# Performance work log

Hardware: AMD Instinct MI355X
Metric: run time of the kernel (lower is better)

## Reference

```python
import jax, jax.numpy as jnp
import numpy as np

QUANTSCALE = 0.25
EPS = 1e-5

def act_quant(x):
    # 8-bit symmetric activation quantization, scale per last dim (as in BitNetMCU)
    scale = 127.0 / jnp.maximum(jnp.max(jnp.abs(x), axis=-1, keepdims=True), EPS)
    return jnp.clip(jnp.round(x * scale), -128.0, 127.0) / scale

def wq_binary(w):
    # Binary weights: sign(w - mean) scaled by mean(|w|) (per-tensor)
    scale = jnp.mean(jnp.abs(w))
    return jnp.sign(w - jnp.mean(w)) * scale

def wq_4bitsym(w):
    # 4-bit symmetric levels {+-0.5,...,+-7.5}/scale, per-tensor scale from mean(|w|)
    mag = jnp.maximum(jnp.mean(jnp.abs(w)), EPS)
    scale = QUANTSCALE * 8.0 / mag
    return (jnp.clip(jnp.round(w * scale - 0.5), -8.0, 7.0) + 0.5) / scale

def ste(x, q):
    # straight-through estimator: forward = q, backward = identity
    return x + jax.lax.stop_gradient(q - x)

def rmsnorm(x):
    return x * jax.lax.rsqrt(jnp.mean(x * x, axis=-1, keepdims=True) + EPS)

def bitlinear(x, w):
    xn = rmsnorm(x)                    # NormType='RMS'
    xq = ste(xn, act_quant(xn))
    wq = ste(w, wq_binary(w))          # QuantType='Binary'
    return xq @ wq.T

def bitconv(x, w, groups):
    # NormType='None', QuantType='4bitsym'
    xq = ste(x, act_quant(x))
    wq = ste(w, wq_4bitsym(w))
    return jax.lax.conv_general_dilated(
        xq, wq, window_strides=(1, 1), padding='VALID',
        dimension_numbers=('NCHW', 'OIHW', 'NCHW'),
        feature_group_count=groups)

def setup_inputs() -> dict:
    key = jax.random.key(0)
    ks = jax.random.split(key, 8)
    B, W1, W2, W3 = 16384, 512, 512, 512
    return {
        'x':        jax.random.normal(ks[0], (B, 1, 16, 16), jnp.float32),
        'conv1_w':  jax.random.normal(ks[1], (16, 1, 3, 3), jnp.float32) * 0.1,
        'conv1b_w': jax.random.normal(ks[2], (16, 1, 3, 3), jnp.float32) * 0.1,
        'conv2_w':  jax.random.normal(ks[3], (96, 1, 12, 12), jnp.float32) * 0.1,
        'fc1_w':    jax.random.normal(ks[4], (W1, 96), jnp.float32) * 0.1,
        'fc2_w':    jax.random.normal(ks[5], (W2, W1), jnp.float32) * 0.1,
        'fc3_w':    jax.random.normal(ks[6], (W3, W2), jnp.float32) * 0.1,
        'fcl_w':    jax.random.normal(ks[7], (10, W3), jnp.float32) * 0.1,
    }

def reference(x, conv1_w, conv1b_w, conv2_w, fc1_w, fc2_w, fc3_w, fcl_w):
    h = jax.nn.relu(bitconv(x, conv1_w, 1))    # [B,16,14,14]
    h = jax.nn.relu(bitconv(h, conv1b_w, 16))  # depthwise -> [B,16,12,12]
    h = jax.nn.relu(bitconv(h, conv2_w, 16))   # grouped k12 -> [B,96,1,1]
    h = h.reshape(h.shape[0], -1)              # [B,96]
    h = jax.nn.relu(bitlinear(h, fc1_w))
    h = jax.nn.relu(bitlinear(h, fc2_w))
    h = jax.nn.relu(bitlinear(h, fc3_w))
    return bitlinear(h, fcl_w)                 # [B,10] logits (dropout is eval no-op)
```

## Files before the change

kernel.cpp:

```cpp
#include <hip/hip_runtime.h>
#include <math.h>

#define EPSQ 1e-5

typedef int v4i  __attribute__((ext_vector_type(4)));
typedef int v16i __attribute__((ext_vector_type(16)));

__device__ void bstat(const float* __restrict__ w, int cnt, double2* dst, int divn) {
    __shared__ double ls[4], la[4];
    int t = threadIdx.x;
    double s = 0.0, a = 0.0;
    const float4* w4 = (const float4*)w;
    int nv = cnt >> 2;
    for (int i = t; i < nv; i += 256) {
        float4 v = w4[i];
        s += (double)v.x + (double)v.y + (double)v.z + (double)v.w;
        a += fabs((double)v.x) + fabs((double)v.y) + fabs((double)v.z) + fabs((double)v.w);
    }
    for (int o = 32; o; o >>= 1) { s += __shfl_down(s, o); a += __shfl_down(a, o); }
    if ((t & 63) == 0) { ls[t >> 6] = s; la[t >> 6] = a; }
    __syncthreads();
    if (t == 0) {
        for (int i = 1; i < 4; i++) { s += ls[i]; a += la[i]; }
        if (divn > 0) { dst->x = s / divn; dst->y = a / divn; }
        else          { dst->x = s;        dst->y = a; }
    }
}

__global__ __launch_bounds__(256) void wstats_part(
    const float* __restrict__ a0, const float* __restrict__ a1,
    const float* __restrict__ a2, const float* __restrict__ a3,
    const float* __restrict__ a4, const float* __restrict__ a5,
    const float* __restrict__ a6, double2* __restrict__ part,
    double2* __restrict__ stats) {
    int b = blockIdx.x;
    if      (b == 0) bstat(a0, 144,   stats + 0, 144);
    else if (b == 1) bstat(a1, 144,   stats + 1, 144);
    else if (b == 2) bstat(a2, 13824, stats + 2, 13824);
    else if (b == 3) bstat(a6, 5120,  stats + 6, 5120);
    else if (b < 8)  bstat(a3 + (b - 4)  * 12288, 12288, part + (b - 4), 0);
    else if (b < 24) bstat(a4 + (b - 8)  * 16384, 16384, part + 4 + (b - 8), 0);
    else             bstat(a5 + (b - 24) * 16384, 16384, part + 20 + (b - 24), 0);
}

__global__ __launch_bounds__(64) void wstats_comb(const double2* __restrict__ part,
                                                  double2* __restrict__ stats) {
    int t = threadIdx.x;
    if (t == 0) {
        double s = 0, a = 0;
        for (int i = 0; i < 4; i++) { s += part[i].x; a += part[i].y; }
        stats[3].x = s / 49152.0; stats[3].y = a / 49152.0;
    } else if (t == 1) {
        double s = 0, a = 0;
        for (int i = 4; i < 20; i++) { s += part[i].x; a += part[i].y; }
        stats[4].x = s / 262144.0; stats[4].y = a / 262144.0;
    } else if (t == 2) {
        double s = 0, a = 0;
        for (int i = 20; i < 36; i++) { s += part[i].x; a += part[i].y; }
        stats[5].x = s / 262144.0; stats[5].y = a / 262144.0;
    }
}

__device__ inline float q4odd(float w, double mag) {
    double sc = 2.0 / fmax(mag, EPSQ);
    double q = fmin(fmax(rint((double)w * sc - 0.5), -8.0), 7.0);
    return (float)(2.0 * q + 1.0);
}

__global__ __launch_bounds__(256) void wq_conv(
    const float* __restrict__ wc1, const float* __restrict__ wc1b,
    const float* __restrict__ wc2, const double2* __restrict__ stats,
    float* __restrict__ c1o, float* __restrict__ c1bo, float* __restrict__ c2o) {
    int i = blockIdx.x * 256 + threadIdx.x;
    if (i < 144) c1o[i] = q4odd(wc1[i], stats[0].y);
    else if (i < 288) c1bo[i - 144] = q4odd(wc1b[i - 144], stats[1].y);
    else if (i < 288 + 13824) { int j = i - 288; c2o[j] = q4odd(wc2[j], stats[2].y); }
}

__device__ inline char bsign(float w, double mean) {
    double d = (double)w - mean;
    return d > 0.0 ? (char)1 : (d < 0.0 ? (char)-1 : (char)0);
}

__global__ __launch_bounds__(256) void wq_fc(
    const float* __restrict__ wfc1, const float* __restrict__ wfc2,
    const float* __restrict__ wfc3, const float* __restrict__ wfcl,
    const double2* __restrict__ stats,
    char* __restrict__ f1, char* __restrict__ f2,
    char* __restrict__ f3, char* __restrict__ fl) {
    int i = blockIdx.x * 256 + threadIdx.x;
    if (i < 65536) {
        int row = i >> 7, k = i & 127;
        f1[i] = (k < 96) ? bsign(wfc1[row * 96 + k], stats[3].x) : (char)0;
        return;
    }
    i -= 65536;
    if (i < 262144) { f2[i] = bsign(wfc2[i], stats[4].x); return; }
    i -= 262144;
    if (i < 262144) { f3[i] = bsign(wfc3[i], stats[5].x); return; }
    i -= 262144;
    if (i < 5120)   { fl[i] = bsign(wfcl[i], stats[6].x); }
}

template <int Wd>
__device__ inline double cpix(const float (&rq)[3][Wd], const float* wv,
                              const double* inv, int qx) {
    float d0 = rq[0][qx] * wv[0] + rq[0][qx + 1] * wv[1] + rq[0][qx + 2] * wv[2];
    float d1 = rq[1][qx] * wv[3] + rq[1][qx + 1] * wv[4] + rq[1][qx + 2] * wv[5];
    float d2 = rq[2][qx] * wv[6] + rq[2][qx + 1] * wv[7] + rq[2][qx + 2] * wv[8];
    return (double)d0 * inv[0] + (double)d1 * inv[1] + (double)d2 * inv[2];
}

__global__ __launch_bounds__(256) void conv_fused(
    const float* __restrict__ x, const float* __restrict__ w1o,
    const float* __restrict__ w1bo, const float* __restrict__ w2o,
    const double2* __restrict__ stats,
    char* __restrict__ xq96, double* __restrict__ arow) {
    __shared__ float sxp[16][17];
    __shared__ double sinv0[16];
    __shared__ float sh1[16][14][15];
    __shared__ double sinv1[16][14];
    __shared__ float sh2[16][12][13];
    __shared__ double sinv2[16][12];
    __shared__ float sw1[144], sw1b[144];
    __shared__ double sh3p[2][96];
    __shared__ double sh3[96];
    __shared__ double srs[2];
    int b = blockIdx.x, t = threadIdx.x;
    double cw1  = fmax(stats[0].y, EPSQ) * 0.25;
    double cw1b = fmax(stats[1].y, EPSQ) * 0.25;
    double cw2  = fmax(stats[2].y, EPSQ) * 0.25;

    float v = x[(size_t)b * 256 + t];
    if (t < 144) { sw1[t] = w1o[t]; sw1b[t] = w1bo[t]; }
    float m = fabsf(v);
    for (int o = 8; o; o >>= 1) m = fmaxf(m, __shfl_xor(m, o));
    double s0 = 127.0 / fmax((double)m, EPSQ);
    sxp[t >> 4][t & 15] = (float)fmin(fmax(rint((double)v * s0), -128.0), 127.0);
    if ((t & 15) == 0) sinv0[t >> 4] = 1.0 / s0;
    __syncthreads();

    if (t < 224) {
        int c = t / 14, r = t % 14;
        float rq[3][16]; double inv[3];
        #pragma unroll
        for (int i = 0; i < 3; i++) {
            inv[i] = sinv0[r + i];
            #pragma unroll
            for (int j = 0; j < 16; j++) rq[i][j] = sxp[r + i][j];
        }
        float wv[9];
        #pragma unroll
        for (int k = 0; k < 9; k++) wv[k] = sw1[c * 9 + k];
        double vals[14]; double mx = 0.0;
        #pragma unroll
        for (int qx = 0; qx < 14; qx++) {
            vals[qx] = fmax(cpix(rq, wv, inv, qx) * cw1, 0.0);
            mx = fmax(mx, vals[qx]);
        }
        double s2 = 127.0 / fmax(mx, EPSQ);
        sinv1[c][r] = 1.0 / s2;
        #pragma unroll
        for (int qx = 0; qx < 14; qx++)
            sh1[c][r][qx] = (float)fmin(fmax(rint(vals[qx] * s2), -128.0), 127.0);
    }
    __syncthreads();

    if (t < 192) {
        int c = t / 12, r = t % 12;
        float rq[3][14]; double inv[3];
        #pragma unroll
        for (int i = 0; i < 3; i++) {
            inv[i] = sinv1[c][r + i];
            #pragma unroll
            for (int j = 0; j < 14; j++) rq[i][j] = sh1[c][r + i][j];
        }
        float wv[9];
        #pragma unroll
        for (int k = 0; k < 9; k++) wv[k] = sw1b[c * 9 + k];
        double vals[12]; double mx = 0.0;
        #pragma unroll
        for (int qx = 0; qx < 12; qx++) {
            vals[qx] = fmax(cpix(rq, wv, inv, qx) * cw1b, 0.0);
            mx = fmax(mx, vals[qx]);
        }
        double s3 = 127.0 / fmax(mx, EPSQ);
        sinv2[c][r] = 1.0 / s3;
        #pragma unroll
        for (int qx = 0; qx < 12; qx++)
            sh2[c][r][qx] = (float)fmin(fmax(rint(vals[qx] * s3), -128.0), 127.0);
    }
    __syncthreads();

    if (t < 192) {
        int o = t % 96, half = t / 96;
        int g = o / 6;
        const float* wk = w2o + o * 144 + half * 72;
        double acc = 0.0;
        #pragma unroll
        for (int hh = 0; hh < 6; hh++) {
            int row = half * 6 + hh;
            float4 w0 = *(const float4*)(wk + hh * 12);
            float4 w1 = *(const float4*)(wk + hh * 12 + 4);
            float4 w2v = *(const float4*)(wk + hh * 12 + 8);
            const float* sr = &sh2[g][row][0];
            float d = 0.f;
            d += sr[0] * w0.x; d += sr[1] * w0.y; d += sr[2] * w0.z; d += sr[3] * w0.w;
            d += sr[4] * w1.x; d += sr[5] * w1.y; d += sr[6] * w1.z; d += sr[7] * w1.w;
            d += sr[8] * w2v.x; d += sr[9] * w2v.y; d += sr[10] * w2v.z; d += sr[11] * w2v.w;
            acc += (double)d * sinv2[g][row];
        }
        sh3p[half][o] = acc;
    }
    __syncthreads();
    if (t < 96) sh3[t] = fmax((sh3p[0][t] + sh3p[1][t]) * cw2, 0.0);
    __syncthreads();

    if (t < 64) {
        double a = sh3[t];
        double bb = (t < 32) ? sh3[64 + t] : 0.0;
        double ss = a * a + bb * bb;
        double mxx = fmax(fabs(a), fabs(bb));
        for (int o = 32; o; o >>= 1) {
            ss += __shfl_down(ss, o);
            mxx = fmax(mxx, __shfl_down(mxx, o));
        }
        if (t == 0) {
            double r = 1.0 / sqrt(ss / 96.0 + 1e-5);
            double s4 = 127.0 / fmax(mxx * r, EPSQ);
            srs[0] = r; srs[1] = s4;
        }
    }
    __syncthreads();
    if (t < 128) {
        char q = 0;
        if (t < 96) {
            double xn = sh3[t] * srs[0];
            q = (char)(int)fmin(fmax(rint(xn * srs[1]), -128.0), 127.0);
        }
        xq96[(size_t)b * 128 + t] = q;
        if (t == 0) arow[b] = 1.0 / srs[1];
    }
}

__global__ __launch_bounds__(256) void gemm_i8(
    const char* __restrict__ Xq, const char* __restrict__ Wq,
    int* __restrict__ h, int N, int K, int dorelu) {
    __shared__ char As[16384];
    __shared__ char Bs[16384];
    int t = threadIdx.x;
    int lane = t & 63;
    int w = t >> 6, wr = w >> 1, wc = w & 1;
    int m0 = blockIdx.y * 128, n0 = blockIdx.x * 128;

    v16i acc[2][2] = {};

    for (int k0 = 0; k0 < K; k0 += 128) {
        #pragma unroll
        for (int p = 0; p < 4; p++) {
            int slot = p * 256 + t;
            int row = slot >> 3;
            int cb = (slot & 7) * 16;
            int4 va = *(const int4*)(Xq + (size_t)(m0 + row) * K + k0 + cb);
            int4 vb = *(const int4*)(Wq + (size_t)(n0 + row) * K + k0 + cb);
            int dst = row * 128 + (cb ^ ((row & 7) << 4));
            *(int4*)(As + dst) = va;
            *(int4*)(Bs + dst) = vb;
        }
        __syncthreads();
        int ra0 = wr * 64 + (lane & 31);
        int rb0 = wc * 64 + (lane & 31);
        int ksel = (lane >> 5) * 16;
        #pragma unroll
        for (int kk = 0; kk < 4; kk++) {
            int kb = kk * 32 + ksel;
            v4i a0 = *(v4i*)(As + ra0 * 128        + (kb ^ ((ra0 & 7) << 4)));
            v4i a1 = *(v4i*)(As + (ra0 + 32) * 128 + (kb ^ ((ra0 & 7) << 4)));
            v4i b0 = *(v4i*)(Bs + rb0 * 128        + (kb ^ ((rb0 & 7) << 4)));
            v4i b1 = *(v4i*)(Bs + (rb0 + 32) * 128 + (kb ^ ((rb0 & 7) << 4)));
            acc[0][0] = __builtin_amdgcn_mfma_i32_32x32x32_i8(a0, b0, acc[0][0], 0, 0, 0);
            acc[0][1] = __builtin_amdgcn_mfma_i32_32x32x32_i8(a0, b1, acc[0][1], 0, 0, 0);
            acc[1][0] = __builtin_amdgcn_mfma_i32_32x32x32_i8(a1, b0, acc[1][0], 0, 0, 0);
            acc[1][1] = __builtin_amdgcn_mfma_i32_32x32x32_i8(a1, b1, acc[1][1], 0, 0, 0);
        }
        __syncthreads();
    }

    #pragma unroll
    for (int mt = 0; mt < 2; mt++) {
        int rbase = m0 + wr * 64 + mt * 32 + 4 * (lane >> 5);
        #pragma unroll
        for (int nt = 0; nt < 2; nt++) {
            int cbase = n0 + wc * 64 + nt * 32 + (lane & 31);
            #pragma unroll
            for (int g = 0; g < 4; g++)
                #pragma unroll
                for (int q = 0; q < 4; q++) {
                    int vv = acc[mt][nt][g * 4 + q];
                    if (dorelu) vv = max(vv, 0);
                    h[(size_t)(rbase + g * 8 + q) * N + cbase] = vv;
                }
        }
    }
}

__global__ __launch_bounds__(256) void rmsq_i8(const int* __restrict__ h,
                                               const double2* __restrict__ stats,
                                               int sidx,
                                               double* __restrict__ arow,
                                               char* __restrict__ xq) {
    __shared__ double wsumd[4];
    __shared__ int wmaxi[4];
    __shared__ double fr[2];
    int b = blockIdx.x, t = threadIdx.x;
    const int* xr = h + (size_t)b * 512;
    int v0 = xr[t], v1 = xr[t + 256];
    double ss = (double)v0 * (double)v0 + (double)v1 * (double)v1;
    int mi = max(abs(v0), abs(v1));
    for (int o = 32; o; o >>= 1) {
        ss += __shfl_down(ss, o);
        mi = max(mi, __shfl_down(mi, o));
    }
    if ((t & 63) == 0) { wsumd[t >> 6] = ss; wmaxi[t >> 6] = mi; }
    __syncthreads();
    if (t == 0) {
        double S = wsumd[0] + wsumd[1] + wsumd[2] + wsumd[3];
        int M = max(max(wmaxi[0], wmaxi[1]), max(wmaxi[2], wmaxi[3]));
        double c = stats[sidx].y * arow[b];
        double mean = S * c * c / 512.0;
        double r = 1.0 / sqrt(mean + 1e-5);
        double s = 127.0 / fmax((double)M * c * r, EPSQ);
        fr[0] = c * r * s;
        fr[1] = s;
    }
    __syncthreads();
    double cs = fr[0];
    char q0 = (char)(int)fmin(fmax(rint((double)v0 * cs), -128.0), 127.0);
    char q1 = (char)(int)fmin(fmax(rint((double)v1 * cs), -128.0), 127.0);
    xq[(size_t)b * 512 + t] = q0;
    xq[(size_t)b * 512 + t + 256] = q1;
    if (t == 0) arow[b] = 1.0 / fr[1];
}

__device__ inline int bdot(int a, int b) {
    int r = ((a << 24) >> 24) * ((b << 24) >> 24);
    r += ((a << 16) >> 24) * ((b << 16) >> 24);
    r += ((a << 8) >> 24) * ((b << 8) >> 24);
    r += (a >> 24) * (b >> 24);
    return r;
}

__global__ __launch_bounds__(256) void fcl_k(const char* __restrict__ Xq,
                                             const char* __restrict__ Wq,
                                             const double* __restrict__ arow,
                                             const double2* __restrict__ stats,
                                             float* __restrict__ out) {
    int gi = blockIdx.x * 256 + threadIdx.x;
    int mrow = gi / 10, n = gi - mrow * 10;
    const int4* xp = (const int4*)(Xq + (size_t)mrow * 512);
    const int4* wp = (const int4*)(Wq + n * 512);
    int acc = 0;
    #pragma unroll 8
    for (int i = 0; i < 32; i++) {
        int4 a = xp[i], b = wp[i];
        acc += bdot(a.x, b.x) + bdot(a.y, b.y) + bdot(a.z, b.z) + bdot(a.w, b.w);
    }
    out[gi] = (float)((double)acc * stats[6].y * arow[mrow]);
}

extern "C" void kernel_launch(void* const* d_in, const int* in_sizes, int n_in,
                              void* d_out, int out_size, void* d_ws, size_t ws_size,
                              hipStream_t stream) {
    const float* x     = (const float*)d_in[0];
    const float* w_c1  = (const float*)d_in[1];
    const float* w_c1b = (const float*)d_in[2];
    const float* w_c2  = (const float*)d_in[3];
    const float* w_fc1 = (const float*)d_in[4];
    const float* w_fc2 = (const float*)d_in[5];
    const float* w_fc3 = (const float*)d_in[6];
    const float* w_fcl = (const float*)d_in[7];
    float* out = (float*)d_out;
    char* wsb = (char*)d_ws;
    const int B = 16384;

    float*   c1o   = (float*)(wsb + 0);
    float*   c1bo  = (float*)(wsb + 1024);
    float*   c2o   = (float*)(wsb + 2048);
    double2* stats = (double2*)(wsb + 57344);
    double2* part  = (double2*)(wsb + 57856);
    char*    f1q   = wsb + 65536;
    char*    f2q   = wsb + 131072;
    char*    f3q   = wsb + 393216;
    char*    flq   = wsb + 655360;
    double*  arow  = (double*)(wsb + 663552);
    char*    xq96  = wsb + 1048576;
    char*    xq512 = wsb + 3145728;
    int*     h     = (int*)(wsb + 11534336);

    wstats_part<<<40, 256, 0, stream>>>(w_c1, w_c1b, w_c2, w_fc1, w_fc2, w_fc3,
                                        w_fcl, part, stats);
    wstats_comb<<<1, 64, 0, stream>>>(part, stats);
    wq_conv<<<56, 256, 0, stream>>>(w_c1, w_c1b, w_c2, stats, c1o, c1bo, c2o);
    wq_fc<<<2324, 256, 0, stream>>>(w_fc1, w_fc2, w_fc3, w_fcl, stats, f1q, f2q, f3q, flq);

    conv_fused<<<B, 256, 0, stream>>>(x, c1o, c1bo, c2o, stats, xq96, arow);

    gemm_i8<<<dim3(4, B / 128), 256, 0, stream>>>(xq96, f1q, h, 512, 128, 1);
    rmsq_i8<<<B, 256, 0, stream>>>(h, stats, 3, arow, xq512);
    gemm_i8<<<dim3(4, B / 128), 256, 0, stream>>>(xq512, f2q, h, 512, 512, 1);
    rmsq_i8<<<B, 256, 0, stream>>>(h, stats, 4, arow, xq512);
    gemm_i8<<<dim3(4, B / 128), 256, 0, stream>>>(xq512, f3q, h, 512, 512, 1);
    rmsq_i8<<<B, 256, 0, stream>>>(h, stats, 5, arow, xq512);
    fcl_k<<<640, 256, 0, stream>>>(xq512, flq, arow, stats, out);
}
```

Before: 292.2 us.

## Fuse int8 FC GEMM with RMSNorm and requantization epilogue per row block

Replaces the separate int8 GEMM plus per-row RMS/quantize kernels with one kernel per layer. Each block computes a full 32x512 output row tile, reduces sum-of-squares and max inside the block, and writes int8 activations directly. This removes the int32 intermediate round trip through global memory and three launches. In exchange every block reloads the whole 512-wide weight tile, occupancy is tied to a 64KB shared buffer, and the layer writes xq512 in place while it is also the input. The change also drops clamps the conv path never needs and folds the conv weight scale into the row inverse scales.

```diff
diff --git a/kernel.cpp b/kernel.cpp
--- a/kernel.cpp
+++ b/kernel.cpp
@@ -136,7 +136,7 @@
     float m = fabsf(v);
     for (int o = 8; o; o >>= 1) m = fmaxf(m, __shfl_xor(m, o));
     double s0 = 127.0 / fmax((double)m, EPSQ);
-    sxp[t >> 4][t & 15] = (float)fmin(fmax(rint((double)v * s0), -128.0), 127.0);
+    sxp[t >> 4][t & 15] = (float)rint((double)v * s0);
     if ((t & 15) == 0) sinv0[t >> 4] = 1.0 / s0;
     __syncthreads();
 
@@ -145,7 +145,7 @@
         float rq[3][16]; double inv[3];
         #pragma unroll
         for (int i = 0; i < 3; i++) {
-            inv[i] = sinv0[r + i];
+            inv[i] = sinv0[r + i] * cw1;
             #pragma unroll
             for (int j = 0; j < 16; j++) rq[i][j] = sxp[r + i][j];
         }
@@ -155,14 +155,14 @@
         double vals[14]; double mx = 0.0;
         #pragma unroll
         for (int qx = 0; qx < 14; qx++) {
-            vals[qx] = fmax(cpix(rq, wv, inv, qx) * cw1, 0.0);
+            vals[qx] = fmax(cpix(rq, wv, inv, qx), 0.0);
             mx = fmax(mx, vals[qx]);
         }
         double s2 = 127.0 / fmax(mx, EPSQ);
         sinv1[c][r] = 1.0 / s2;
         #pragma unroll
         for (int qx = 0; qx < 14; qx++)
-            sh1[c][r][qx] = (float)fmin(fmax(rint(vals[qx] * s2), -128.0), 127.0);
+            sh1[c][r][qx] = (float)rint(vals[qx] * s2);
     }
     __syncthreads();
 
@@ -171,7 +171,7 @@
         float rq[3][14]; double inv[3];
         #pragma unroll
         for (int i = 0; i < 3; i++) {
-            inv[i] = sinv1[c][r + i];
+            inv[i] = sinv1[c][r + i] * cw1b;
             #pragma unroll
             for (int j = 0; j < 14; j++) rq[i][j] = sh1[c][r + i][j];
         }
@@ -181,14 +181,14 @@
         double vals[12]; double mx = 0.0;
         #pragma unroll
         for (int qx = 0; qx < 12; qx++) {
-            vals[qx] = fmax(cpix(rq, wv, inv, qx) * cw1b, 0.0);
+            vals[qx] = fmax(cpix(rq, wv, inv, qx), 0.0);
             mx = fmax(mx, vals[qx]);
         }
         double s3 = 127.0 / fmax(mx, EPSQ);
         sinv2[c][r] = 1.0 / s3;
         #pragma unroll
         for (int qx = 0; qx < 12; qx++)
-            sh2[c][r][qx] = (float)fmin(fmax(rint(vals[qx] * s3), -128.0), 127.0);
+            sh2[c][r][qx] = (float)rint(vals[qx] * s3);
     }
     __syncthreads();
 
@@ -236,110 +236,113 @@
         char q = 0;
         if (t < 96) {
             double xn = sh3[t] * srs[0];
-            q = (char)(int)fmin(fmax(rint(xn * srs[1]), -128.0), 127.0);
+            q = (char)(int)rint(xn * srs[1]);
         }
         xq96[(size_t)b * 128 + t] = q;
         if (t == 0) arow[b] = 1.0 / srs[1];
     }
 }
 
-__global__ __launch_bounds__(256) void gemm_i8(
-    const char* __restrict__ Xq, const char* __restrict__ Wq,
-    int* __restrict__ h, int N, int K, int dorelu) {
-    __shared__ char As[16384];
-    __shared__ char Bs[16384];
+__global__ __launch_bounds__(256, 2) void fc_fused(
+    const char* __restrict__ Xq, const char* __restrict__ Wq, int K,
+    const double2* __restrict__ stats, int sidx,
+    double* __restrict__ arow, char* __restrict__ xq) {
+    __shared__ char As[32 * 128];
+    __shared__ char Bs[512 * 128];
+    __shared__ double redS[4][32];
+    __shared__ int    redM[4][32];
+    __shared__ double csrow[32];
     int t = threadIdx.x;
     int lane = t & 63;
-    int w = t >> 6, wr = w >> 1, wc = w & 1;
-    int m0 = blockIdx.y * 128, n0 = blockIdx.x * 128;
-
-    v16i acc[2][2] = {};
+    int w = t >> 6;
+    int m0 = blockIdx.x * 32;
+
+    v16i acc[4] = {};
 
     for (int k0 = 0; k0 < K; k0 += 128) {
-        #pragma unroll
-        for (int p = 0; p < 4; p++) {
+        {
+            int row = t >> 3, cb = (t & 7) * 16;
+            *(int4*)(As + row * 128 + (cb ^ ((row & 7) << 4))) =
+                *(const int4*)(Xq + (size_t)(m0 + row) * K + k0 + cb);
+        }
+        #pragma unroll
+        for (int p = 0; p < 16; p++) {
             int slot = p * 256 + t;
-            int row = slot >> 3;
-            int cb = (slot & 7) * 16;
-            int4 va = *(const int4*)(Xq + (size_t)(m0 + row) * K + k0 + cb);
-            int4 vb = *(const int4*)(Wq + (size_t)(n0 + row) * K + k0 + cb);
-            int dst = row * 128 + (cb ^ ((row & 7) << 4));
-            *(int4*)(As + dst) = va;
-            *(int4*)(Bs + dst) = vb;
+            int row = slot >> 3, cb = (slot & 7) * 16;
+            *(int4*)(Bs + row * 128 + (cb ^ ((row & 7) << 4))) =
+                *(const int4*)(Wq + (size_t)row * K + k0 + cb);
         }
         __syncthreads();
-        int ra0 = wr * 64 + (lane & 31);
-        int rb0 = wc * 64 + (lane & 31);
+        int ra = lane & 31;
         int ksel = (lane >> 5) * 16;
         #pragma unroll
         for (int kk = 0; kk < 4; kk++) {
             int kb = kk * 32 + ksel;
-            v4i a0 = *(v4i*)(As + ra0 * 128        + (kb ^ ((ra0 & 7) << 4)));
-            v4i a1 = *(v4i*)(As + (ra0 + 32) * 128 + (kb ^ ((ra0 & 7) << 4)));
-            v4i b0 = *(v4i*)(Bs + rb0 * 128        + (kb ^ ((rb0 & 7) << 4)));
-            v4i b1 = *(v4i*)(Bs + (rb0 + 32) * 128 + (kb ^ ((rb0 & 7) << 4)));
-            acc[0][0] = __builtin_amdgcn_mfma_i32_32x32x32_i8(a0, b0, acc[0][0], 0, 0, 0);
-            acc[0][1] = __builtin_amdgcn_mfma_i32_32x32x32_i8(a0, b1, acc[0][1], 0, 0, 0);
-            acc[1][0] = __builtin_amdgcn_mfma_i32_32x32x32_i8(a1, b0, acc[1][0], 0, 0, 0);
-            acc[1][1] = __builtin_amdgcn_mfma_i32_32x32x32_i8(a1, b1, acc[1][1], 0, 0, 0);
+            v4i a = *(v4i*)(As + ra * 128 + (kb ^ ((ra & 7) << 4)));
+            #pragma unroll
+            for (int nt = 0; nt < 4; nt++) {
+                int rb = w * 128 + nt * 32 + (lane & 31);
+                v4i bb = *(v4i*)(Bs + rb * 128 + (kb ^ ((rb & 7) << 4)));
+                acc[nt] = __builtin_amdgcn_mfma_i32_32x32x32_i8(a, bb, acc[nt], 0, 0, 0);
+            }
         }
         __syncthreads();
     }
 
+    double ps[16]; int pm[16];
     #pragma unroll
-    for (int mt = 0; mt < 2; mt++) {
-        int rbase = m0 + wr * 64 + mt * 32 + 4 * (lane >> 5);
-        #pragma unroll
-        for (int nt = 0; nt < 2; nt++) {
-            int cbase = n0 + wc * 64 + nt * 32 + (lane & 31);
-            #pragma unroll
-            for (int g = 0; g < 4; g++)
-                #pragma unroll
-                for (int q = 0; q < 4; q++) {
-                    int vv = acc[mt][nt][g * 4 + q];
-                    if (dorelu) vv = max(vv, 0);
-                    h[(size_t)(rbase + g * 8 + q) * N + cbase] = vv;
-                }
-        }
-    }
-}
-
-__global__ __launch_bounds__(256) void rmsq_i8(const int* __restrict__ h,
-                                               const double2* __restrict__ stats,
-                                               int sidx,
-                                               double* __restrict__ arow,
-                                               char* __restrict__ xq) {
-    __shared__ double wsumd[4];
-    __shared__ int wmaxi[4];
-    __shared__ double fr[2];
-    int b = blockIdx.x, t = threadIdx.x;
-    const int* xr = h + (size_t)b * 512;
-    int v0 = xr[t], v1 = xr[t + 256];
-    double ss = (double)v0 * (double)v0 + (double)v1 * (double)v1;
-    int mi = max(abs(v0), abs(v1));
-    for (int o = 32; o; o >>= 1) {
-        ss += __shfl_down(ss, o);
-        mi = max(mi, __shfl_down(mi, o));
-    }
-    if ((t & 63) == 0) { wsumd[t >> 6] = ss; wmaxi[t >> 6] = mi; }
-    __syncthreads();
-    if (t == 0) {
-        double S = wsumd[0] + wsumd[1] + wsumd[2] + wsumd[3];
-        int M = max(max(wmaxi[0], wmaxi[1]), max(wmaxi[2], wmaxi[3]));
-        double c = stats[sidx].y * arow[b];
+    for (int reg = 0; reg < 16; reg++) {
+        int v0 = max(acc[0][reg], 0), v1 = max(acc[1][reg], 0);
+        int v2 = max(acc[2][reg], 0), v3 = max(acc[3][reg], 0);
+        acc[0][reg] = v0; acc[1][reg] = v1; acc[2][reg] = v2; acc[3][reg] = v3;
+        ps[reg] = (double)v0 * v0 + (double)v1 * v1 + (double)v2 * v2 + (double)v3 * v3;
+        pm[reg] = max(max(v0, v1), max(v2, v3));
+    }
+    #pragma unroll
+    for (int o = 1; o < 32; o <<= 1) {
+        #pragma unroll
+        for (int reg = 0; reg < 16; reg++) {
+            ps[reg] += __shfl_xor(ps[reg], o);
+            pm[reg] = max(pm[reg], __shfl_xor(pm[reg], o));
+        }
+    }
+    if ((lane & 31) == 0) {
+        int h = lane >> 5;
+        #pragma unroll
+        for (int reg = 0; reg < 16; reg++) {
+            int row = (reg & 3) + 8 * (reg >> 2) + 4 * h;
+            redS[w][row] = ps[reg];
+            redM[w][row] = pm[reg];
+        }
+    }
+    __syncthreads();
+    if (t < 32) {
+        double S = redS[0][t] + redS[1][t] + redS[2][t] + redS[3][t];
+        int M = max(max(redM[0][t], redM[1][t]), max(redM[2][t], redM[3][t]));
+        double c = stats[sidx].y * arow[m0 + t];
         double mean = S * c * c / 512.0;
         double r = 1.0 / sqrt(mean + 1e-5);
         double s = 127.0 / fmax((double)M * c * r, EPSQ);
-        fr[0] = c * r * s;
-        fr[1] = s;
-    }
-    __syncthreads();
-    double cs = fr[0];
-    char q0 = (char)(int)fmin(fmax(rint((double)v0 * cs), -128.0), 127.0);
-    char q1 = (char)(int)fmin(fmax(rint((double)v1 * cs), -128.0), 127.0);
-    xq[(size_t)b * 512 + t] = q0;
-    xq[(size_t)b * 512 + t + 256] = q1;
-    if (t == 0) arow[b] = 1.0 / fr[1];
+        csrow[t] = c * r * s;
+        arow[m0 + t] = 1.0 / s;
+    }
+    __syncthreads();
+
+    #pragma unroll
+    for (int nt = 0; nt < 4; nt++) {
+        int col = w * 128 + nt * 32 + (lane & 31);
+        #pragma unroll
+        for (int reg = 0; reg < 16; reg++) {
+            int row = (reg & 3) + 8 * (reg >> 2) + 4 * (lane >> 5);
+            Bs[row * 512 + col] = (char)(int)rint((double)acc[nt][reg] * csrow[row]);
+        }
+    }
+    __syncthreads();
+    #pragma unroll
+    for (int i = 0; i < 4; i++) {
+        int idx = i * 256 + t;
+        *(int4*)(xq + (size_t)m0 * 512 + idx * 16) = *(const int4*)(Bs + idx * 16);
+    }
 }
 
 __device__ inline int bdot(int a, int b) {
@@ -395,7 +398,6 @@
     double*  arow  = (double*)(wsb + 663552);
     char*    xq96  = wsb + 1048576;
     char*    xq512 = wsb + 3145728;
-    int*     h     = (int*)(wsb + 11534336);
 
     wstats_part<<<40, 256, 0, stream>>>(w_c1, w_c1b, w_c2, w_fc1, w_fc2, w_fc3,
                                         w_fcl, part, stats);
@@ -405,11 +407,9 @@
 
     conv_fused<<<B, 256, 0, stream>>>(x, c1o, c1bo, c2o, stats, xq96, arow);
 
-    gemm_i8<<<dim3(4, B / 128), 256, 0, stream>>>(xq96, f1q, h, 512, 128, 1);
-    rmsq_i8<<<B, 256, 0, stream>>>(h, stats, 3, arow, xq512);
-    gemm_i8<<<dim3(4, B / 128), 256, 0, stream>>>(xq512, f2q, h, 512, 512, 1);
-    rmsq_i8<<<B, 256, 0, stream>>>(h, stats, 4, arow, xq512);
-    gemm_i8<<<dim3(4, B / 128), 256, 0, stream>>>(xq512, f3q, h, 512, 512, 1);
-    rmsq_i8<<<B, 256, 0, stream>>>(h, stats, 5, arow, xq512);
+    fc_fused<<<B / 32, 256, 0, stream>>>(xq96,  f1q, 128, stats, 3, arow, xq512);
+    fc_fused<<<B / 32, 256, 0, stream>>>(xq512, f2q, 512, stats, 4, arow, xq512);
+    fc_fused<<<B / 32, 256, 0, stream>>>(xq512, f3q, 512, stats, 5, arow, xq512);
+
     fcl_k<<<640, 256, 0, stream>>>(xq512, flq, arow, stats, out);
 }
```

Measured after the change: 247.3 us. 15.4% less time.
